# Performance work log

Hardware: AMD Instinct MI355X
Metric: run time of the kernel (lower is better)

## Reference

```python
import jax, jax.numpy as jnp
import numpy as np

B, S, D, H = 2, 2048, 1024, 16
DK = D // H


def setup_inputs() -> dict:
    key = jax.random.key(0)
    ks = jax.random.split(key, 12)
    init = lambda k, shp: (jax.random.normal(k, shp, dtype=jnp.float32) * 0.02)
    return {
        'query': jax.random.normal(ks[0], (B, S, D), dtype=jnp.float32),
        'key_in': jax.random.normal(ks[1], (B, S, D), dtype=jnp.float32),
        'value': jax.random.normal(ks[2], (B, S, D), dtype=jnp.float32),
        'w_q': init(ks[3], (D, D)), 'b_q': jnp.zeros((D,), jnp.float32),
        'w_k': init(ks[4], (D, D)), 'b_k': jnp.zeros((D,), jnp.float32),
        'w_v': init(ks[5], (D, D)), 'b_v': jnp.zeros((D,), jnp.float32),
        'w_o': init(ks[6], (D, D)), 'b_o': jnp.zeros((D,), jnp.float32),
        'fuzzy_centers': jax.random.normal(ks[7], (H, 3), dtype=jnp.float32),
        'fuzzy_widths': jnp.ones((H, 3), jnp.float32),
        'temperature': jnp.ones((1,), jnp.float32),
    }


def reference(query, key_in, value, w_q, b_q, w_k, b_k, w_v, b_v, w_o, b_o,
              fuzzy_centers, fuzzy_widths, temperature):
    b, s, d = query.shape
    h, dk = H, DK
    proj = lambda x, w, bias: x @ w.T + bias
    # [b,s,d] -> [b,h,s,dk]
    Q = proj(query, w_q, b_q).reshape(b, s, h, dk).transpose(0, 2, 1, 3)
    K = proj(key_in, w_k, b_k).reshape(b, s, h, dk).transpose(0, 2, 1, 3)
    V = proj(value, w_v, b_v).reshape(b, s, h, dk).transpose(0, 2, 1, 3)
    scores = jnp.einsum('bhsd,bhtd->bhst', Q, K) / np.sqrt(dk).astype(np.float32)
    # Faithful to torch: every (head,func) gaussian is applied to ALL heads' scores,
    # so each score gets sum of h*3 memberships, divided by 3.
    c = fuzzy_centers.reshape(-1)
    w = fuzzy_widths.reshape(-1)
    fz = jnp.zeros_like(scores)
    for i in range(h * 3):  # small fixed loop over membership functions
        fz = fz + jnp.exp(-(scores - c[i]) ** 2 / (2.0 * w[i] ** 2))
    fz = (fz / 3.0) / temperature[0]
    attn = jax.nn.softmax(fz, axis=-1)
    attended = jnp.einsum('bhst,bhtd->bhsd', attn, V)
    attended = attended.transpose(0, 2, 1, 3).reshape(b, s, d)
    return attended @ w_o.T + b_o
```

## Files before the change

kernel.cpp:

```cpp
#include <hip/hip_runtime.h>
#include <hip/hip_bf16.h>


#define S_LEN 2048
#define DMODEL 1024
#define NHEAD 16
#define DKH 64
#define NLUT 2048
#define LUT_MIN (-10.0f)
#define LUT_MAX (10.0f)

typedef __attribute__((ext_vector_type(8))) short bfx8;
typedef __attribute__((ext_vector_type(4))) float fx4;
typedef __attribute__((ext_vector_type(16))) float fx16;
typedef __attribute__((ext_vector_type(4))) unsigned ux4;

__device__ __forceinline__ short f2bf(float x) {
    unsigned u = __builtin_bit_cast(unsigned, x);
    u = (u + 0x7fffu + ((u >> 16) & 1u)) >> 16;
    return (short)u;
}

__device__ __forceinline__ unsigned cvt_pk_bf16(float lo, float hi) {
    unsigned r;
    asm("v_cvt_pk_bf16_f32 %0, %1, %2" : "=v"(r) : "v"(lo), "v"(hi));
    return r;
}

__device__ __forceinline__ void plane_swap(unsigned& a, unsigned& b) {
    asm volatile("v_permlane32_swap_b32 %0, %1" : "+v"(a), "+v"(b));
}

__device__ __forceinline__ void stage8_f32(const float* __restrict__ src, short* dst) {
    float4 a = *(const float4*)(src);
    float4 b = *(const float4*)(src + 4);
    bfx8 r;
    r[0] = f2bf(a.x); r[1] = f2bf(a.y); r[2] = f2bf(a.z); r[3] = f2bf(a.w);
    r[4] = f2bf(b.x); r[5] = f2bf(b.y); r[6] = f2bf(b.z); r[7] = f2bf(b.w);
    *(bfx8*)dst = r;
}

__device__ __forceinline__ void gload_lds16(const void* g, void* l) {
    __builtin_amdgcn_global_load_lds(
        (const __attribute__((address_space(1))) unsigned int*)g,
        (__attribute__((address_space(3))) unsigned int*)l, 16, 0, 0);
}

__device__ void lut_body(const float* __restrict__ centers, const float* __restrict__ widths,
                         const float* __restrict__ temp, unsigned* __restrict__ lutp) {
    __shared__ float fzb[NLUT];
    __shared__ float red[256];
    __shared__ float cs[48], wsb[48];
    int tid = threadIdx.x;
    if (tid < 48) { cs[tid] = centers[tid]; wsb[tid] = widths[tid]; }
    __syncthreads();
    float invT = 1.0f / temp[0];
    const float step = (LUT_MAX - LUT_MIN) / (float)(NLUT - 1);
    float lmax = -1e30f;
    for (int i = tid; i < NLUT; i += 256) {
        float s = LUT_MIN + step * (float)i;
        float fz = 0.0f;
        #pragma unroll 1
        for (int j = 0; j < 48; j++) {
            float d = s - cs[j];
            float w = wsb[j];
            fz += expf(-(d * d) / (2.0f * w * w));
        }
        fz = fz * (1.0f / 3.0f) * invT;
        fzb[i] = fz;
        lmax = fmaxf(lmax, fz);
    }
    red[tid] = lmax;
    __syncthreads();
    for (int off = 128; off > 0; off >>= 1) {
        if (tid < off) red[tid] = fmaxf(red[tid], red[tid + off]);
        __syncthreads();
    }
    float m = red[0];
    __syncthreads();
    for (int i = tid; i < NLUT; i += 256) fzb[i] = expf(fzb[i] - m);
    __syncthreads();
    for (int i = tid; i < NLUT; i += 256) {
        float g0 = fzb[i];
        float g1 = fzb[(i + 1 < NLUT) ? i + 1 : NLUT - 1];
        unsigned lo = (unsigned short)f2bf(g0);
        unsigned hi = (unsigned short)f2bf(g1);
        lutp[i] = lo | (hi << 16);
    }
}

__global__ void build_lut_pk(const float* centers, const float* widths,
                             const float* temp, unsigned* lutp) {
    lut_body(centers, widths, temp, lutp);
}

__global__ void cast_bf16(const float* __restrict__ src, short* __restrict__ dst, int n8) {
    int i = blockIdx.x * 256 + threadIdx.x;
    if (i < n8) stage8_f32(src + (size_t)i * 8, dst + (size_t)i * 8);
}

__global__ void prep_all(const float* q, const float* kin, const float* v,
        const float* wq, const float* wk, const float* wv, const float* wo,
        short* xq, short* xk, short* xv,
        short* bwq, short* bwk, short* bwv, short* bwo,
        const float* centers, const float* widths, const float* temp,
        unsigned* lutp) {
    int bid = blockIdx.x;
    if (bid >= 8192) {
        lut_body(centers, widths, temp, lutp);
        return;
    }
    const float* src; short* dst; int blk;
    if (bid < 6144) {
        int y = bid >> 11; blk = bid & 2047;
        src = (y == 0) ? q : (y == 1) ? kin : v;
        dst = (y == 0) ? xq : (y == 1) ? xk : xv;
    } else {
        int y = (bid - 6144) >> 9; blk = (bid - 6144) & 511;
        src = (y == 0) ? wq : (y == 1) ? wk : (y == 2) ? wv : wo;
        dst = (y == 0) ? bwq : (y == 1) ? bwk : (y == 2) ? bwv : bwo;
    }
    size_t i = (size_t)blk * 256 + threadIdx.x;
    stage8_f32(src + i * 8, (short*)dst + i * 8);
}

struct GemmJob {
    const short* A; const short* W; const float* bias;
    short* obf; float* of32; int mode; float scale;
};

__global__ __launch_bounds__(256, 2) void gemm128(GemmJob j0, GemmJob j1, GemmJob j2) {
    __shared__ __align__(16) short As[2][128 * 32];
    __shared__ __align__(16) short Bs[2][128 * 32];
    GemmJob jb = (blockIdx.z == 0) ? j0 : (blockIdx.z == 1) ? j1 : j2;
    int tid = threadIdx.x, wave = tid >> 6, lane = tid & 63, quad = lane >> 4, l15 = lane & 15;
    int m0 = blockIdx.y * 128, n0 = blockIdx.x * 128;
    int wm = (wave >> 1) * 64, wn = (wave & 1) * 64;

    fx4 acc[4][4];
    #pragma unroll
    for (int i = 0; i < 4; i++)
        #pragma unroll
        for (int j = 0; j < 4; j++)
            #pragma unroll
            for (int r = 0; r < 4; r++) acc[i][j][r] = 0.0f;

    int fc = (quad ^ ((l15 >> 1) & 3)) * 8;

    int srow[2], sgc[2];
    #pragma unroll
    for (int r = 0; r < 2; r++) {
        int slot = r * 256 + wave * 64 + lane;
        srow[r] = slot >> 2;
        sgc[r] = (slot & 3) ^ ((srow[r] >> 1) & 3);
    }

    auto stage = [&](int k0, int buf) {
        #pragma unroll
        for (int r = 0; r < 2; r++) {
            gload_lds16(jb.A + (size_t)(m0 + srow[r]) * DMODEL + k0 + sgc[r] * 8,
                        &As[buf][(r * 256 + wave * 64) * 8]);
            gload_lds16(jb.W + (size_t)(n0 + srow[r]) * DMODEL + k0 + sgc[r] * 8,
                        &Bs[buf][(r * 256 + wave * 64) * 8]);
        }
    };

    stage(0, 0);
    __syncthreads();
    int buf = 0;
    for (int k0 = 0; k0 < DMODEL; k0 += 32) {
        if (k0 + 32 < DMODEL) stage(k0 + 32, buf ^ 1);
        bfx8 af[4], bfr[4];
        #pragma unroll
        for (int i = 0; i < 4; i++) af[i] = *(const bfx8*)(&As[buf][(wm + i * 16 + l15) * 32 + fc]);
        #pragma unroll
        for (int j = 0; j < 4; j++) bfr[j] = *(const bfx8*)(&Bs[buf][(wn + j * 16 + l15) * 32 + fc]);
        #pragma unroll
        for (int i = 0; i < 4; i++)
            #pragma unroll
            for (int j = 0; j < 4; j++)
                acc[i][j] = __builtin_amdgcn_mfma_f32_16x16x32_bf16(af[i], bfr[j], acc[i][j], 0, 0, 0);
        __syncthreads();
        buf ^= 1;
    }

    #pragma unroll
    for (int j = 0; j < 4; j++) {
        int n = n0 + wn + j * 16 + l15;
        float bv = jb.bias[n];
        #pragma unroll
        for (int i = 0; i < 4; i++) {
            #pragma unroll
            for (int r = 0; r < 4; r++) {
                int m = m0 + wm + i * 16 + quad * 4 + r;
                float v = (acc[i][j][r] + bv) * jb.scale;
                if (jb.mode == 0) {
                    int b = m >> 11, s = m & 2047, h = n >> 6, dk = n & 63;
                    jb.obf[(((size_t)(b * NHEAD + h)) * S_LEN + s) * DKH + dk] = f2bf(v);
                } else if (jb.mode == 1) {
                    int b = m >> 11, s = m & 2047, h = n >> 6, dk = n & 63;
                    jb.obf[(((size_t)(b * NHEAD + h)) * DKH + dk) * S_LEN + s] = f2bf(v);
                } else {
                    jb.of32[(size_t)m * DMODEL + n] = v;
                }
            }
        }
    }
}

__global__ __launch_bounds__(256, 4) void flash_fuzzy(const short* __restrict__ Qb,
        const short* __restrict__ Kb, const short* __restrict__ VTb,
        const unsigned* __restrict__ lutg, short* __restrict__ AO) {
    __shared__ __align__(16) short Ks[2][64 * 64];
    __shared__ __align__(16) short Vs[2][64 * 64];
    __shared__ unsigned lut[NLUT];

    int tid = threadIdx.x, wave = tid >> 6, lane = tid & 63;
    int l31 = lane & 31, hi = lane >> 5;
    int wq = wave >> 1, st = wave & 1;
    int q0 = blockIdx.x * 64, bh = blockIdx.y;
    const short* Qp = Qb + (size_t)bh * S_LEN * DKH;
    const short* Kp = Kb + (size_t)bh * S_LEN * DKH;
    const short* Vp = VTb + (size_t)bh * DKH * S_LEN;

    int srow[2], sgc[2];
    #pragma unroll
    for (int r = 0; r < 2; r++) {
        int slot = (wave * 2 + r) * 64 + lane;
        srow[r] = slot >> 3;
        sgc[r] = (slot & 7) ^ (srow[r] & 7);
    }
    auto stage = [&](int t0, int buf) {
        #pragma unroll
        for (int r = 0; r < 2; r++) {
            gload_lds16(Kp + (size_t)(t0 + srow[r]) * DKH + sgc[r] * 8,
                        &Ks[buf][((wave * 2 + r) * 64) * 8]);
            gload_lds16(Vp + (size_t)srow[r] * S_LEN + t0 + sgc[r] * 8,
                        &Vs[buf][((wave * 2 + r) * 64) * 8]);
        }
    };

    stage(0, 0);

    #pragma unroll
    for (int i = tid; i < NLUT / 4; i += 256)
        ((uint4*)lut)[i] = ((const uint4*)lutg)[i];

    bfx8 aq[4];
    #pragma unroll
    for (int ks = 0; ks < 4; ks++)
        aq[ks] = *(const bfx8*)(Qp + (size_t)(q0 + wq * 32 + l31) * DKH + ks * 16 + hi * 8);

    fx16 oacc[2];
    #pragma unroll
    for (int dt = 0; dt < 2; dt++)
        #pragma unroll
        for (int r = 0; r < 16; r++) oacc[dt][r] = 0.0f;
    float den = 0.0f;

    const float invh = (float)(NLUT - 1) / (LUT_MAX - LUT_MIN);
    const float xoff = -LUT_MIN * invh;

    __syncthreads();
    int buf = 0;
    for (int t0 = 0; t0 < S_LEN; t0 += 64) {
        if (t0 + 64 < S_LEN) stage(t0 + 64, buf ^ 1);

        fx16 sac;
        #pragma unroll
        for (int r = 0; r < 16; r++) sac[r] = 0.0f;
        {
            int row = st * 32 + l31;
            #pragma unroll
            for (int ks = 0; ks < 4; ks++) {
                bfx8 kf = *(const bfx8*)(&Ks[buf][row * 64 + (((ks * 2 + hi) ^ (row & 7)) * 8)]);
                sac = __builtin_amdgcn_mfma_f32_32x32x16_bf16(kf, aq[ks], sac, 0, 0, 0);
            }
        }

        unsigned w[8];
        #pragma unroll
        for (int t = 0; t < 8; t++) {
            float pv[2];
            #pragma unroll
            for (int u = 0; u < 2; u++) {
                float s = sac[t * 2 + u];
                float x = fmaf(s, invh, xoff);
                x = fminf(fmaxf(x, 0.0f), (float)(NLUT - 1));
                int j = (int)x;
                float f = x - (float)j;
                unsigned pr = lut[j];
                float v0 = __builtin_bit_cast(float, pr << 16);
                float v1 = __builtin_bit_cast(float, pr & 0xffff0000u);
                pv[u] = fmaf(f, v1 - v0, v0);
            }
            w[t] = cvt_pk_bf16(pv[0], pv[1]);
        }
        #pragma unroll
        for (int t = 0; t < 8; t++) {
            den += __builtin_bit_cast(float, w[t] << 16);
            den += __builtin_bit_cast(float, w[t] & 0xffff0000u);
        }

        plane_swap(w[0], w[2]); plane_swap(w[1], w[3]);
        plane_swap(w[4], w[6]); plane_swap(w[5], w[7]);
        ux4 b0v = {w[0], w[1], w[2], w[3]};
        ux4 b1v = {w[4], w[5], w[6], w[7]};
        bfx8 pb0 = __builtin_bit_cast(bfx8, b0v);
        bfx8 pb1 = __builtin_bit_cast(bfx8, b1v);

        #pragma unroll
        for (int dt = 0; dt < 2; dt++) {
            int row = dt * 32 + l31;
            bfx8 v0f = *(const bfx8*)(&Vs[buf][row * 64 + (((st * 4 + 0 + hi) ^ (row & 7)) * 8)]);
            bfx8 v1f = *(const bfx8*)(&Vs[buf][row * 64 + (((st * 4 + 2 + hi) ^ (row & 7)) * 8)]);
            oacc[dt] = __builtin_amdgcn_mfma_f32_32x32x16_bf16(v0f, pb0, oacc[dt], 0, 0, 0);
            oacc[dt] = __builtin_amdgcn_mfma_f32_32x32x16_bf16(v1f, pb1, oacc[dt], 0, 0, 0);
        }

        __syncthreads();
        buf ^= 1;
    }

    den += __shfl_xor(den, 32);

    float* obuf = (float*)Ks + wq * 2048;
    float* dbuf = (float*)lut;
    if (st == 1) {
        #pragma unroll
        for (int dt = 0; dt < 2; dt++)
            #pragma unroll
            for (int r = 0; r < 16; r++)
                obuf[(dt * 16 + r) * 64 + lane] = oacc[dt][r];
        dbuf[wq * 64 + lane] = den;
    }
    __syncthreads();
    if (st == 0) {
        float dtot = den + dbuf[wq * 64 + lane];
        int b = bh >> 4, h = bh & 15;
        #pragma unroll
        for (int dt = 0; dt < 2; dt++) {
            #pragma unroll
            for (int r = 0; r < 16; r++) {
                float o = oacc[dt][r] + obuf[(dt * 16 + r) * 64 + lane];
                int dk = dt * 32 + (r & 3) + 8 * (r >> 2) + 4 * hi;
                int q = q0 + wq * 32 + l31;
                AO[((size_t)(b * S_LEN + q)) * DMODEL + h * DKH + dk] = f2bf(o / dtot);
            }
        }
    }
}

extern "C" void kernel_launch(void* const* d_in, const int* in_sizes, int n_in,
                              void* d_out, int out_size, void* d_ws, size_t ws_size,
                              hipStream_t stream) {
    const float* query   = (const float*)d_in[0];
    const float* key_in  = (const float*)d_in[1];
    const float* value   = (const float*)d_in[2];
    const float* w_q     = (const float*)d_in[3];
    const float* b_q     = (const float*)d_in[4];
    const float* w_k     = (const float*)d_in[5];
    const float* b_k     = (const float*)d_in[6];
    const float* w_v     = (const float*)d_in[7];
    const float* b_v     = (const float*)d_in[8];
    const float* w_o     = (const float*)d_in[9];
    const float* b_o     = (const float*)d_in[10];
    const float* centers = (const float*)d_in[11];
    const float* widths  = (const float*)d_in[12];
    const float* temp    = (const float*)d_in[13];

    char* p = (char*)d_ws;
    auto alloc = [&](size_t bytes) -> void* {
        void* r = (void*)p;
        p += (bytes + 255) & ~(size_t)255;
        return r;
    };
    const size_t nBHSD = (size_t)2 * NHEAD * S_LEN * DKH;
    const size_t nW    = (size_t)DMODEL * DMODEL;
    unsigned* lutp = (unsigned*)alloc(NLUT * 4);
    short* Qb  = (short*)alloc(nBHSD * 2);
    short* Kb  = (short*)alloc(nBHSD * 2);
    short* VTb = (short*)alloc(nBHSD * 2);

    char* save = p;
    short* xq  = (short*)alloc(nBHSD * 2);
    short* xk  = (short*)alloc(nBHSD * 2);
    short* xv  = (short*)alloc(nBHSD * 2);
    short* bwq = (short*)alloc(nW * 2);
    short* bwk = (short*)alloc(nW * 2);
    short* bwv = (short*)alloc(nW * 2);
    short* bwo = (short*)alloc(nW * 2);
    bool fused = ((size_t)(p - (char*)d_ws) <= ws_size);

    dim3 blk(256);
    dim3 gq(8, 32, 3), g1(8, 32, 1), fg(32, 32);
    GemmJob JO;

    if (fused) {
        short* AO = xq;
        prep_all<<<dim3(8193), blk, 0, stream>>>(query, key_in, value, w_q, w_k, w_v, w_o,
                xq, xk, xv, bwq, bwk, bwv, bwo, centers, widths, temp, lutp);
        GemmJob JQ = {xq, bwq, b_q, Qb,  nullptr, 0, 0.125f};
        GemmJob JK = {xk, bwk, b_k, Kb,  nullptr, 0, 1.0f};
        GemmJob JV = {xv, bwv, b_v, VTb, nullptr, 1, 1.0f};
        gemm128<<<gq, blk, 0, stream>>>(JQ, JK, JV);
        flash_fuzzy<<<fg, blk, 0, stream>>>(Qb, Kb, VTb, lutp, AO);
        JO = {AO, bwo, b_o, nullptr, (float*)d_out, 2, 1.0f};
        gemm128<<<g1, blk, 0, stream>>>(JO, JO, JO);
    } else {
        p = save;
        short* xf = (short*)alloc(nBHSD * 2);
        short* wb = (short*)alloc(nW * 2);
        short* AO = xf;
        const int n8x = (int)(nBHSD / 8), n8w = (int)(nW / 8);
        dim3 cg((n8x + 255) / 256), cw((n8w + 255) / 256);
        build_lut_pk<<<dim3(1), blk, 0, stream>>>(centers, widths, temp, lutp);
        cast_bf16<<<cg, blk, 0, stream>>>(query, xf, n8x);
        cast_bf16<<<cw, blk, 0, stream>>>(w_q, wb, n8w);
        JO = {xf, wb, b_q, Qb, nullptr, 0, 0.125f};
        gemm128<<<g1, blk, 0, stream>>>(JO, JO, JO);
        cast_bf16<<<cg, blk, 0, stream>>>(key_in, xf, n8x);
        cast_bf16<<<cw, blk, 0, stream>>>(w_k, wb, n8w);
        JO = {xf, wb, b_k, Kb, nullptr, 0, 1.0f};
        gemm128<<<g1, blk, 0, stream>>>(JO, JO, JO);
        cast_bf16<<<cg, blk, 0, stream>>>(value, xf, n8x);
        cast_bf16<<<cw, blk, 0, stream>>>(w_v, wb, n8w);
        JO = {xf, wb, b_v, VTb, nullptr, 1, 1.0f};
        gemm128<<<g1, blk, 0, stream>>>(JO, JO, JO);
        flash_fuzzy<<<fg, blk, 0, stream>>>(Qb, Kb, VTb, lutp, AO);
        cast_bf16<<<cw, blk, 0, stream>>>(w_o, wb, n8w);
        JO = {AO, wb, b_o, nullptr, (float*)d_out, 2, 1.0f};
        gemm128<<<g1, blk, 0, stream>>>(JO, JO, JO);
    }
}
```

Baseline: 308.3 us.

## Use fp32 slope LUT, MFMA row sums, single-buffered KV, gemm occupancy 3

The fuzzy LUT now stores fp32 value and slope pairs, so interpolation becomes one fma with no bf16 unpacking, and clamping uses med3. The softmax denominator is accumulated with an extra MFMA against a ones vector in place of scalar adds. K/V staging drops double buffering and uses one buffer with two barriers per tile. The LDS saved goes to the larger fp32 LUT. The GEMM launch-bounds occupancy hint goes from 2 to 3. Losing the prefetch overlap in the flash loop may expose global load latency.

```diff
diff --git a/kernel.cpp b/kernel.cpp
--- a/kernel.cpp
+++ b/kernel.cpp
@@ -47,7 +47,7 @@
 }
 
 __device__ void lut_body(const float* __restrict__ centers, const float* __restrict__ widths,
-                         const float* __restrict__ temp, unsigned* __restrict__ lutp) {
+                         const float* __restrict__ temp, float2* __restrict__ lutf) {
     __shared__ float fzb[NLUT];
     __shared__ float red[256];
     __shared__ float cs[48], wsb[48];
@@ -83,15 +83,13 @@
     for (int i = tid; i < NLUT; i += 256) {
         float g0 = fzb[i];
         float g1 = fzb[(i + 1 < NLUT) ? i + 1 : NLUT - 1];
-        unsigned lo = (unsigned short)f2bf(g0);
-        unsigned hi = (unsigned short)f2bf(g1);
-        lutp[i] = lo | (hi << 16);
+        lutf[i] = make_float2(g0, g1 - g0);
     }
 }
 
 __global__ void build_lut_pk(const float* centers, const float* widths,
-                             const float* temp, unsigned* lutp) {
-    lut_body(centers, widths, temp, lutp);
+                             const float* temp, float2* lutf) {
+    lut_body(centers, widths, temp, lutf);
 }
 
 __global__ void cast_bf16(const float* __restrict__ src, short* __restrict__ dst, int n8) {
@@ -104,10 +102,10 @@
         short* xq, short* xk, short* xv,
         short* bwq, short* bwk, short* bwv, short* bwo,
         const float* centers, const float* widths, const float* temp,
-        unsigned* lutp) {
+        float2* lutf) {
     int bid = blockIdx.x;
     if (bid >= 8192) {
-        lut_body(centers, widths, temp, lutp);
+        lut_body(centers, widths, temp, lutf);
         return;
     }
     const float* src; short* dst; int blk;
@@ -129,7 +127,7 @@
     short* obf; float* of32; int mode; float scale;
 };
 
-__global__ __launch_bounds__(256, 2) void gemm128(GemmJob j0, GemmJob j1, GemmJob j2) {
+__global__ __launch_bounds__(256, 3) void gemm128(GemmJob j0, GemmJob j1, GemmJob j2) {
     __shared__ __align__(16) short As[2][128 * 32];
     __shared__ __align__(16) short Bs[2][128 * 32];
     GemmJob jb = (blockIdx.z == 0) ? j0 : (blockIdx.z == 1) ? j1 : j2;
@@ -210,10 +208,10 @@
 
 __global__ __launch_bounds__(256, 4) void flash_fuzzy(const short* __restrict__ Qb,
         const short* __restrict__ Kb, const short* __restrict__ VTb,
-        const unsigned* __restrict__ lutg, short* __restrict__ AO) {
-    __shared__ __align__(16) short Ks[2][64 * 64];
-    __shared__ __align__(16) short Vs[2][64 * 64];
-    __shared__ unsigned lut[NLUT];
+        const float2* __restrict__ lutg, short* __restrict__ AO) {
+    __shared__ __align__(16) short Ks[64 * 64];
+    __shared__ __align__(16) short Vs[64 * 64];
+    __shared__ __align__(16) float2 lutf[NLUT];
 
     int tid = threadIdx.x, wave = tid >> 6, lane = tid & 63;
     int l31 = lane & 31, hi = lane >> 5;
@@ -223,6 +221,31 @@
     const short* Kp = Kb + (size_t)bh * S_LEN * DKH;
     const short* Vp = VTb + (size_t)bh * DKH * S_LEN;
 
+    #pragma unroll
+    for (int i = tid; i < NLUT / 2; i += 256)
+        ((float4*)lutf)[i] = ((const float4*)lutg)[i];
+
+    bfx8 aq[4];
+    #pragma unroll
+    for (int ks = 0; ks < 4; ks++)
+        aq[ks] = *(const bfx8*)(Qp + (size_t)(q0 + wq * 32 + l31) * DKH + ks * 16 + hi * 8);
+
+    bfx8 ones;
+    #pragma unroll
+    for (int i = 0; i < 8; i++) ones[i] = (short)0x3F80;
+
+    fx16 oacc[2];
+    fx16 dacc;
+    #pragma unroll
+    for (int r = 0; r < 16; r++) dacc[r] = 0.0f;
+    #pragma unroll
+    for (int dt = 0; dt < 2; dt++)
+        #pragma unroll
+        for (int r = 0; r < 16; r++) oacc[dt][r] = 0.0f;
+
+    const float invh = (float)(NLUT - 1) / (LUT_MAX - LUT_MIN);
+    const float xoff = -LUT_MIN * invh;
+
     int srow[2], sgc[2];
     #pragma unroll
     for (int r = 0; r < 2; r++) {
@@ -230,41 +253,17 @@
         srow[r] = slot >> 3;
         sgc[r] = (slot & 7) ^ (srow[r] & 7);
     }
-    auto stage = [&](int t0, int buf) {
+
+    for (int t0 = 0; t0 < S_LEN; t0 += 64) {
+        __syncthreads();
         #pragma unroll
         for (int r = 0; r < 2; r++) {
             gload_lds16(Kp + (size_t)(t0 + srow[r]) * DKH + sgc[r] * 8,
-                        &Ks[buf][((wave * 2 + r) * 64) * 8]);
+                        &Ks[((wave * 2 + r) * 64) * 8]);
             gload_lds16(Vp + (size_t)srow[r] * S_LEN + t0 + sgc[r] * 8,
-                        &Vs[buf][((wave * 2 + r) * 64) * 8]);
-        }
-    };
-
-    stage(0, 0);
-
-    #pragma unroll
-    for (int i = tid; i < NLUT / 4; i += 256)
-        ((uint4*)lut)[i] = ((const uint4*)lutg)[i];
-
-    bfx8 aq[4];
-    #pragma unroll
-    for (int ks = 0; ks < 4; ks++)
-        aq[ks] = *(const bfx8*)(Qp + (size_t)(q0 + wq * 32 + l31) * DKH + ks * 16 + hi * 8);
-
-    fx16 oacc[2];
-    #pragma unroll
-    for (int dt = 0; dt < 2; dt++)
-        #pragma unroll
-        for (int r = 0; r < 16; r++) oacc[dt][r] = 0.0f;
-    float den = 0.0f;
-
-    const float invh = (float)(NLUT - 1) / (LUT_MAX - LUT_MIN);
-    const float xoff = -LUT_MIN * invh;
-
-    __syncthreads();
-    int buf = 0;
-    for (int t0 = 0; t0 < S_LEN; t0 += 64) {
-        if (t0 + 64 < S_LEN) stage(t0 + 64, buf ^ 1);
+                        &Vs[((wave * 2 + r) * 64) * 8]);
+        }
+        __syncthreads();
 
         fx16 sac;
         #pragma unroll
@@ -273,7 +272,7 @@
             int row = st * 32 + l31;
             #pragma unroll
             for (int ks = 0; ks < 4; ks++) {
-                bfx8 kf = *(const bfx8*)(&Ks[buf][row * 64 + (((ks * 2 + hi) ^ (row & 7)) * 8)]);
+                bfx8 kf = *(const bfx8*)(&Ks[row * 64 + (((ks * 2 + hi) ^ (row & 7)) * 8)]);
                 sac = __builtin_amdgcn_mfma_f32_32x32x16_bf16(kf, aq[ks], sac, 0, 0, 0);
             }
         }
@@ -286,20 +285,13 @@
             for (int u = 0; u < 2; u++) {
                 float s = sac[t * 2 + u];
                 float x = fmaf(s, invh, xoff);
-                x = fminf(fmaxf(x, 0.0f), (float)(NLUT - 1));
+                x = __builtin_amdgcn_fmed3f(x, 0.0f, (float)(NLUT - 1));
                 int j = (int)x;
-                float f = x - (float)j;
-                unsigned pr = lut[j];
-                float v0 = __builtin_bit_cast(float, pr << 16);
-                float v1 = __builtin_bit_cast(float, pr & 0xffff0000u);
-                pv[u] = fmaf(f, v1 - v0, v0);
+                float f = x - floorf(x);
+                float2 pr = lutf[j];
+                pv[u] = fmaf(f, pr.y, pr.x);
             }
             w[t] = cvt_pk_bf16(pv[0], pv[1]);
-        }
-        #pragma unroll
-        for (int t = 0; t < 8; t++) {
-            den += __builtin_bit_cast(float, w[t] << 16);
-            den += __builtin_bit_cast(float, w[t] & 0xffff0000u);
         }
 
         plane_swap(w[0], w[2]); plane_swap(w[1], w[3]);
@@ -312,20 +304,20 @@
         #pragma unroll
         for (int dt = 0; dt < 2; dt++) {
             int row = dt * 32 + l31;
-            bfx8 v0f = *(const bfx8*)(&Vs[buf][row * 64 + (((st * 4 + 0 + hi) ^ (row & 7)) * 8)]);
-            bfx8 v1f = *(const bfx8*)(&Vs[buf][row * 64 + (((st * 4 + 2 + hi) ^ (row & 7)) * 8)]);
+            bfx8 v0f = *(const bfx8*)(&Vs[row * 64 + (((st * 4 + 0 + hi) ^ (row & 7)) * 8)]);
+            bfx8 v1f = *(const bfx8*)(&Vs[row * 64 + (((st * 4 + 2 + hi) ^ (row & 7)) * 8)]);
             oacc[dt] = __builtin_amdgcn_mfma_f32_32x32x16_bf16(v0f, pb0, oacc[dt], 0, 0, 0);
             oacc[dt] = __builtin_amdgcn_mfma_f32_32x32x16_bf16(v1f, pb1, oacc[dt], 0, 0, 0);
         }
-
-        __syncthreads();
-        buf ^= 1;
-    }
-
-    den += __shfl_xor(den, 32);
-
-    float* obuf = (float*)Ks + wq * 2048;
-    float* dbuf = (float*)lut;
+        dacc = __builtin_amdgcn_mfma_f32_32x32x16_bf16(ones, pb0, dacc, 0, 0, 0);
+        dacc = __builtin_amdgcn_mfma_f32_32x32x16_bf16(ones, pb1, dacc, 0, 0, 0);
+    }
+
+    float den = dacc[0];
+
+    __syncthreads();
+    float* obuf = (wq == 0) ? (float*)Ks : (float*)Vs;
+    float* dbuf = (float*)lutf;
     if (st == 1) {
         #pragma unroll
         for (int dt = 0; dt < 2; dt++)
@@ -377,7 +369,7 @@
     };
     const size_t nBHSD = (size_t)2 * NHEAD * S_LEN * DKH;
     const size_t nW    = (size_t)DMODEL * DMODEL;
-    unsigned* lutp = (unsigned*)alloc(NLUT * 4);
+    float2* lutp = (float2*)alloc(NLUT * 8);
     short* Qb  = (short*)alloc(nBHSD * 2);
     short* Kb  = (short*)alloc(nBHSD * 2);
     short* VTb = (short*)alloc(nBHSD * 2);
```

After: 301.1 us. 2.3% less time.
